# Kernel optimization log

Hardware: AMD Instinct MI355X
Metric: run time of the kernel (lower is better)

## Reference

```python
import jax, jax.numpy as jnp
import numpy as np

B, S, D, H, DK, F = 8, 1024, 1024, 16, 64, 4096
EPS = 1e-5


def _layer_norm(x, g, b):
    mu = jnp.mean(x, axis=-1, keepdims=True)
    var = jnp.var(x, axis=-1, keepdims=True)
    return (x - mu) * jax.lax.rsqrt(var + EPS) * g + b


def setup_inputs() -> dict:
    key = jax.random.key(0)
    ks = jax.random.split(key, 16)
    s = lambda fan: 1.0 / np.sqrt(fan)
    return {
        "src": jax.random.normal(ks[0], (B, S, D), dtype=jnp.float32),
        "Wq": jax.random.uniform(ks[1], (H, D, DK), jnp.float32, -s(D), s(D)),
        "bq": jnp.zeros((H, DK), jnp.float32),
        "Wk": jax.random.uniform(ks[2], (H, D, DK), jnp.float32, -s(D), s(D)),
        "bk": jnp.zeros((H, DK), jnp.float32),
        "Wv": jax.random.uniform(ks[3], (H, D, DK), jnp.float32, -s(D), s(D)),
        "bv": jnp.zeros((H, DK), jnp.float32),
        "Wo": jax.random.uniform(ks[4], (H * DK, D), jnp.float32, -s(H * DK), s(H * DK)),
        "bo": jnp.zeros((D,), jnp.float32),
        "g1": jnp.ones((D,), jnp.float32),
        "be1": jnp.zeros((D,), jnp.float32),
        "W1": jax.random.uniform(ks[5], (D, F), jnp.float32, -s(D), s(D)),
        "b1": jnp.zeros((F,), jnp.float32),
        "W2": jax.random.uniform(ks[6], (F, D), jnp.float32, -s(F), s(F)),
        "b2": jnp.zeros((D,), jnp.float32),
        "g2": jnp.ones((D,), jnp.float32),
        "be2": jnp.zeros((D,), jnp.float32),
    }


def reference(src, Wq, bq, Wk, bk, Wv, bv, Wo, bo, g1, be1, W1, b1, W2, b2, g2, be2):
    # Per-head projections (vectorized over the Python head loop of the original)
    q = jnp.einsum("bsd,hdk->bhsk", src, Wq) + bq[:, None, :]
    k = jnp.einsum("bsd,hdk->bhsk", src, Wk) + bk[:, None, :]
    v = jnp.einsum("bsd,hdk->bhsk", src, Wv) + bv[:, None, :]
    scale = 1.0 / jnp.sqrt(jnp.asarray(DK, src.dtype))
    scores = jnp.einsum("bhsk,bhtk->bhst", q, k) * scale  # [B,H,S,S]
    attn = jax.nn.softmax(scores, axis=-1)
    o = jnp.einsum("bhst,bhtk->bhsk", attn, v)
    # torch.cat over heads on last dim -> [B,S,H*DK] with head-major feature order
    o = o.transpose(0, 2, 1, 3).reshape(B, S, H * DK)
    attn_out = o @ Wo + bo
    x = _layer_norm(src + attn_out, g1, be1)  # dropout inactive at inference
    ff = jax.nn.relu(x @ W1 + b1) @ W2 + b2
    return _layer_norm(x + ff, g2, be2)
```

## Files before the change

kernel.cpp:

```cpp
#include <hip/hip_runtime.h>

#define Bq 8
#define Sq 1024
#define Dq 1024
#define Hq 16
#define DKq 64
#define Fq 4096
#define TOK (Bq*Sq)

typedef unsigned short u16;
typedef unsigned int u32;
typedef __bf16 bf16x8 __attribute__((ext_vector_type(8)));
typedef float  f32x4  __attribute__((ext_vector_type(4)));

__device__ __forceinline__ float bf2f(u16 u) {
  u32 x = ((u32)u) << 16;
  float f; __builtin_memcpy(&f, &x, 4); return f;
}
__device__ __forceinline__ u16 f2bf(float f) {
  u32 u; __builtin_memcpy(&u, &f, 4);
  u += 0x7fffu + ((u >> 16) & 1u);
  return (u16)(u >> 16);
}
__device__ __forceinline__ void async16(const u16* g, u16* l) {
  __builtin_amdgcn_global_load_lds(
      (__attribute__((address_space(1))) void*)(g),
      (__attribute__((address_space(3))) void*)(l), 16, 0, 0);
}
__device__ __forceinline__ u16 load_in(const void* p, long idx, u32 fp32) {
  return fp32 ? f2bf(((const float*)p)[idx]) : ((const u16*)p)[idx];
}
__device__ __forceinline__ int swzb(int row, int colb) {
  return row * 128 + (colb ^ ((row & 7) << 4));
}

struct InTab { const void* p[17]; int n[17]; };

__global__ void detect_all(InTab tab, u32* flags) {
  __shared__ int sh[3][256];
  int bi = blockIdx.x;
  const u16* buf = (const u16*)tab.p[bi];
  long n = tab.n[bi];
  long m = n < 65536 ? n : 65536;
  int t = threadIdx.x;
  int nanpat = 0, evz = 0, oddnz = 0;
  for (long i = t; i < m; i += 256) {
    u16 v = buf[i];
    if ((v & 0x7F80u) == 0x7F80u) nanpat++;
    if ((i & 1) == 0) { if (v == 0) evz++; }
    else { if (v != 0) oddnz++; }
  }
  sh[0][t] = nanpat; sh[1][t] = evz; sh[2][t] = oddnz;
  __syncthreads();
  for (int s = 128; s > 0; s >>= 1) {
    if (t < s) { sh[0][t] += sh[0][t+s]; sh[1][t] += sh[1][t+s]; sh[2][t] += sh[2][t+s]; }
    __syncthreads();
  }
  if (t == 0) {
    long half = m / 2;
    bool fp32 = (sh[0][0] > 8) ||
                (sh[1][0] > (half * 9) / 10 && sh[2][0] > (half * 9) / 10);
    flags[bi] = fp32 ? 1u : 0u;
  }
}

__global__ void diag_ws_too_small(u16* out, float code) { out[0] = f2bf(code); }

__global__ void diag_mixed(const u32* flags, void* out) {
  u32 a = flags[0];
  if (flags[1] != a || flags[7] != a || flags[11] != a || flags[13] != a) {
    if (a) ((float*)out)[0] = 3000.0f;
    else ((u16*)out)[0] = f2bf(3000.0f);
  }
}

__global__ __launch_bounds__(256) void pack_all(const void* __restrict__ Wq,
                                                const void* __restrict__ Wk,
                                                const void* __restrict__ Wv,
                                                const void* __restrict__ Wo,
                                                const void* __restrict__ W1,
                                                const void* __restrict__ W2,
                                                u16* __restrict__ Wqkv_t,
                                                u16* __restrict__ Wo_t,
                                                u16* __restrict__ W1_t,
                                                u16* __restrict__ W2_t,
                                                const u32* __restrict__ flags) {
  int id = blockIdx.x;
  const void* in; u16* out; u32 f; int R, C; long zin; int r0, c0;
  if (id < 768) {
    int w = id >> 8, t = id & 255;
    int z = t >> 4, xt = t & 15;
    in = (w == 0) ? Wq : ((w == 1) ? Wk : Wv);
    f = flags[(w == 0) ? 1 : ((w == 1) ? 3 : 5)];
    R = 1024; C = 64;
    zin = (long)z * 65536;
    out = Wqkv_t + (long)w * 1048576 + (long)z * 65536;
    r0 = xt * 64; c0 = 0;
  } else if (id < 1024) {
    int t = id - 768; int xt = t & 15, yt = t >> 4;
    in = Wo; f = flags[7]; R = 1024; C = 1024; zin = 0; out = Wo_t;
    r0 = xt * 64; c0 = yt * 64;
  } else if (id < 2048) {
    int t = id - 1024; int xt = t & 15, yt = t >> 4;
    in = W1; f = flags[11]; R = 1024; C = 4096; zin = 0; out = W1_t;
    r0 = xt * 64; c0 = yt * 64;
  } else {
    int t = id - 2048; int xt = t & 63, yt = t >> 6;
    in = W2; f = flags[13]; R = 4096; C = 1024; zin = 0; out = W2_t;
    r0 = xt * 64; c0 = yt * 64;
  }
  __shared__ u16 tile[64][65];
  int tx = threadIdx.x & 63, ty = threadIdx.x >> 6;
#pragma unroll
  for (int it = 0; it < 16; it++) {
    int row = it * 4 + ty;
    tile[row][tx] = load_in(in, zin + (long)(r0 + row) * C + (c0 + tx), f);
  }
  __syncthreads();
#pragma unroll
  for (int it = 0; it < 16; it++) {
    int cc = it * 4 + ty;
    out[(long)(c0 + cc) * R + r0 + tx] = tile[tx][cc];
  }
}

struct CvtTab { const void* p[10]; int flagidx[10]; int dstoff[10]; int n[10]; };
__global__ void cvt_small(CvtTab tab, u16* __restrict__ dst, const u32* __restrict__ flags) {
  int e = blockIdx.x;
  u32 f = flags[tab.flagidx[e]];
  const void* p = tab.p[e];
  int n = tab.n[e], o = tab.dstoff[e];
  for (int i = threadIdx.x; i < n; i += 256) dst[o + i] = load_in(p, i, f);
}

__global__ __launch_bounds__(256) void cvt_src(const void* __restrict__ in,
                                               u16* __restrict__ out,
                                               const u32* __restrict__ flag) {
  u32 f = *flag;
  long i8 = ((long)blockIdx.x * 256 + threadIdx.x) * 8;
  if (f) {
    const float4* f4 = (const float4*)((const float*)in + i8);
    float4 a = f4[0], b = f4[1];
    u16 v[8] = {f2bf(a.x), f2bf(a.y), f2bf(a.z), f2bf(a.w),
                f2bf(b.x), f2bf(b.y), f2bf(b.z), f2bf(b.w)};
    *(uint4*)(out + i8) = *(const uint4*)v;
  } else {
    *(uint4*)(out + i8) = *(const uint4*)((const u16*)in + i8);
  }
}

__global__ __launch_bounds__(256) void gemm_bt(const u16* __restrict__ A,
                                               const u16* __restrict__ Bt,
                                               const u16* __restrict__ bias,
                                               u16* __restrict__ C,
                                               int M, int N, int K, int act) {
  __shared__ alignas(16) u16 sA[2][128 * 32];
  __shared__ alignas(16) u16 sB[2][128 * 32];
  const int tid = threadIdx.x;
  const int wv = tid >> 6, lane = tid & 63;
  const int m16 = lane & 15, quad = lane >> 4;
  const long bm = (long)blockIdx.x * 128;
  const long bn = (long)blockIdx.y * 128;
  const int wm = (wv >> 1) * 64, wn = (wv & 1) * 64;

  f32x4 acc[4][4];
#pragma unroll
  for (int i = 0; i < 4; i++)
#pragma unroll
    for (int j = 0; j < 4; j++) acc[i][j] = (f32x4){0.f, 0.f, 0.f, 0.f};

  const int row_s = tid >> 2;
  const int col_s = (tid & 3) * 8;
  const u16* gA0 = A + (bm + row_s) * (long)K + col_s;
  const u16* gA1 = gA0 + 64 * (long)K;
  const u16* gB0 = Bt + (bn + row_s) * (long)K + col_s;
  const u16* gB1 = gB0 + 64 * (long)K;

  auto stage = [&](int p, int k) {
    async16(gA0 + k, &sA[p][wv * 512]);
    async16(gA1 + k, &sA[p][2048 + wv * 512]);
    async16(gB0 + k, &sB[p][wv * 512]);
    async16(gB1 + k, &sB[p][2048 + wv * 512]);
  };
  auto compute = [&](int p) {
    bf16x8 af[4], bf_[4];
#pragma unroll
    for (int mi = 0; mi < 4; mi++)
      af[mi] = *(const bf16x8*)&sA[p][(wm + mi * 16 + m16) * 32 + quad * 8];
#pragma unroll
    for (int ni = 0; ni < 4; ni++)
      bf_[ni] = *(const bf16x8*)&sB[p][(wn + ni * 16 + m16) * 32 + quad * 8];
#pragma unroll
    for (int mi = 0; mi < 4; mi++)
#pragma unroll
      for (int ni = 0; ni < 4; ni++)
        acc[mi][ni] = __builtin_amdgcn_mfma_f32_16x16x32_bf16(af[mi], bf_[ni], acc[mi][ni], 0, 0, 0);
  };

  stage(0, 0);
  for (int k0 = 0; k0 < K; k0 += 64) {
    __syncthreads();
    if (k0 + 32 < K) stage(1, k0 + 32);
    compute(0);
    __syncthreads();
    if (k0 + 64 < K) stage(0, k0 + 64);
    compute(1);
  }

  float bv4[4];
#pragma unroll
  for (int ni = 0; ni < 4; ni++) bv4[ni] = bf2f(bias[bn + wn + ni * 16 + m16]);

#pragma unroll
  for (int mi = 0; mi < 4; mi++) {
#pragma unroll
    for (int ni = 0; ni < 4; ni++) {
      long col = bn + wn + ni * 16 + m16;
#pragma unroll
      for (int r = 0; r < 4; r++) {
        long row = bm + wm + mi * 16 + quad * 4 + r;
        float v = acc[mi][ni][r] + bv4[ni];
        if (act) v = fmaxf(v, 0.f);
        C[row * N + col] = f2bf(v);
      }
    }
  }
}

#define MF16 __builtin_amdgcn_mfma_f32_16x16x32_bf16

#define TILE256(BUF, NBUF, DOA, DOB, KA, KB, VMS)                              \
  {                                                                            \
                   \
    _Pragma("unroll") for (int mi = 0; mi < 4; mi++)                           \
      _Pragma("unroll") for (int kk = 0; kk < 2; kk++)                         \
        afr[mi][kk] = *(const bf16x8*)&sA[BUF][offA + mi * 1024 + kof[kk]];    \
    _Pragma("unroll") for (int ni = 0; ni < 2; ni++)                           \
      _Pragma("unroll") for (int kk = 0; kk < 2; kk++)                         \
        bfr[ni][kk] = *(const bf16x8*)&sB[BUF][offB + ni * 1024 + kof[kk]];    \
    if (DOA) stA(NBUF, 0, KA);                                                 \
    __builtin_amdgcn_s_barrier();                                              \
    __builtin_amdgcn_s_setprio(1);                                             \
    _Pragma("unroll") for (int kk = 0; kk < 2; kk++)                           \
      _Pragma("unroll") for (int mi = 0; mi < 4; mi++)                         \
        _Pragma("unroll") for (int ni = 0; ni < 2; ni++)                       \
          acc[mi][ni] = MF16(afr[mi][kk], bfr[ni][kk], acc[mi][ni], 0, 0, 0);  \
    __builtin_amdgcn_s_setprio(0);                                             \
    __builtin_amdgcn_s_barrier();                                              \
                                 \
    _Pragma("unroll") for (int ni = 0; ni < 2; ni++)                           \
      _Pragma("unroll") for (int kk = 0; kk < 2; kk++)                         \
        bfr[2 + ni][kk] = *(const bf16x8*)&sB[BUF][offB + (2 + ni) * 1024 + kof[kk]]; \
    if (DOA) stA(NBUF, 1, KA);                                                 \
    __builtin_amdgcn_s_barrier();                                              \
    __builtin_amdgcn_s_setprio(1);                                             \
    _Pragma("unroll") for (int kk = 0; kk < 2; kk++)                           \
      _Pragma("unroll") for (int mi = 0; mi < 4; mi++)                         \
        _Pragma("unroll") for (int ni = 0; ni < 2; ni++)                       \
          acc[mi][2 + ni] = MF16(afr[mi][kk], bfr[2 + ni][kk], acc[mi][2 + ni], 0, 0, 0); \
    __builtin_amdgcn_s_setprio(0);                                             \
    __builtin_amdgcn_s_barrier();                                              \
     \
    _Pragma("unroll") for (int mi = 0; mi < 4; mi++)                           \
      _Pragma("unroll") for (int kk = 0; kk < 2; kk++)                         \
        afr[mi][kk] = *(const bf16x8*)&sA[BUF][offA + (4 + mi) * 1024 + kof[kk]]; \
    if (DOB) stB(BUF, 0, KB);                                                  \
    __builtin_amdgcn_s_barrier();                                              \
    __builtin_amdgcn_s_setprio(1);                                             \
    _Pragma("unroll") for (int kk = 0; kk < 2; kk++)                           \
      _Pragma("unroll") for (int mi = 0; mi < 4; mi++)                         \
        _Pragma("unroll") for (int ni = 0; ni < 2; ni++)                       \
          acc[4 + mi][2 + ni] = MF16(afr[mi][kk], bfr[2 + ni][kk], acc[4 + mi][2 + ni], 0, 0, 0); \
    __builtin_amdgcn_s_setprio(0);                                             \
    __builtin_amdgcn_s_barrier();                                              \
           \
    if (DOB) stB(BUF, 1, KB);                                                  \
    asm volatile("s_waitcnt vmcnt(" VMS ")" ::: "memory");                     \
    __builtin_amdgcn_s_barrier();                                              \
    __builtin_amdgcn_s_setprio(1);                                             \
    _Pragma("unroll") for (int kk = 0; kk < 2; kk++)                           \
      _Pragma("unroll") for (int mi = 0; mi < 4; mi++)                         \
        _Pragma("unroll") for (int ni = 0; ni < 2; ni++)                       \
          acc[4 + mi][ni] = MF16(afr[mi][kk], bfr[ni][kk], acc[4 + mi][ni], 0, 0, 0); \
    __builtin_amdgcn_s_setprio(0);                                             \
    __builtin_amdgcn_s_barrier();                                              \
  }

__global__ __launch_bounds__(512, 2) void gemm256(const u16* __restrict__ A,
                                                  const u16* __restrict__ Bt,
                                                  const u16* __restrict__ bias,
                                                  u16* __restrict__ C,
                                                  int M, int N, int K, int act,
                                                  int ldc, u16* __restrict__ Vt,
                                                  int mode) {
  __shared__ alignas(16) u16 sA[2][16384];
  __shared__ alignas(16) u16 sB[2][16384];
  const int tid = threadIdx.x;
  const int wv = tid >> 6, lane = tid & 63;
  const int m16 = lane & 15, quad = lane >> 4;
  const int wr = wv >> 2, wc = wv & 3;

  const int NT = N >> 8;
  int bid = blockIdx.x;
  {
    const int nwg = gridDim.x;
    const int q = nwg >> 3, r = nwg & 7;
    const int xcd = bid & 7, lp = bid >> 3;
    bid = (xcd < r ? xcd * (q + 1) : r * (q + 1) + (xcd - r) * q) + lp;
  }
  const long bm = (long)(bid / NT) * 256;
  const long bn = (long)(bid % NT) * 256;

  const int r0 = wv * 16 + (lane >> 3);
  const int cstg = ((lane & 7) ^ (lane >> 3)) * 8;
  const u16* gA0 = A  + (bm + r0) * (long)K + cstg;
  const u16* gA1 = A  + (bm + 128 + r0) * (long)K + cstg;
  const u16* gB0 = Bt + (bn + r0) * (long)K + cstg;
  const u16* gB1 = Bt + (bn + 128 + r0) * (long)K + cstg;
  const long k8 = 8 * (long)K;

  auto stA = [&](int nb, int h, int k0) {
    const u16* s = (h ? gA1 : gA0) + k0;
    u16* d = &sA[nb][h * 8192 + wv * 1024];
    async16(s, d);
    async16(s + k8, d + 512);
  };
  auto stB = [&](int nb, int h, int k0) {
    const u16* s = (h ? gB1 : gB0) + k0;
    u16* d = &sB[nb][h * 8192 + wv * 1024];
    async16(s, d);
    async16(s + k8, d + 512);
  };

  const int qs = quad ^ (m16 & 3);
  const int hb = (m16 >> 2) & 1;
  const int kof[2] = {hb * 32, 32 - hb * 32};
  const int offA = wr * 8192 + m16 * 64 + qs * 8;
  const int offB = (wc >> 1) * 8192 + (wc & 1) * 4096 + m16 * 64 + qs * 8;

  f32x4 acc[8][4];
#pragma unroll
  for (int i = 0; i < 8; i++)
#pragma unroll
    for (int j = 0; j < 4; j++) acc[i][j] = (f32x4){0.f, 0.f, 0.f, 0.f};
  bf16x8 afr[4][2], bfr[4][2];

  const int KT = K >> 6;

  stA(0, 0, 0); stA(0, 1, 0); stB(0, 0, 0); stB(0, 1, 0);
  stB(1, 0, 64); stB(1, 1, 64);
  asm volatile("s_waitcnt vmcnt(4)" ::: "memory");
  __builtin_amdgcn_s_barrier();

  int T = 0;
  for (; T + 2 < KT; T += 2) {
    const int kA1 = (T + 1) << 6, kB2 = (T + 2) << 6, kB3 = (T + 3) << 6;
    TILE256(0, 1, true, true, kA1, kB2, "4");
    TILE256(1, 0, true, true, kB2, kB3, "4");
  }
  {
    const int kA1 = (T + 1) << 6;
    TILE256(0, 1, true, false, kA1, 0, "0");
    TILE256(1, 0, false, false, 0, 0, "0");
  }

  float bv4[4];
#pragma unroll
  for (int ni = 0; ni < 4; ni++) bv4[ni] = bf2f(bias[bn + wc * 64 + ni * 16 + m16]);

#pragma unroll
  for (int mi = 0; mi < 8; mi++) {
#pragma unroll
    for (int ni = 0; ni < 4; ni++) {
      long col = bn + wc * 64 + ni * 16 + m16;
      long rowb = bm + wr * 128 + mi * 16 + quad * 4;
      if (mode == 1 && col >= 2048) {
        int hh = ((int)col >> 6) & 15, dk = (int)col & 63;
        int bb = (int)(rowb >> 10), ss = (int)(rowb & 1023);
        u16 t4[4];
#pragma unroll
        for (int r = 0; r < 4; r++) t4[r] = f2bf(acc[mi][ni][r] + bv4[ni]);
        *(uint2*)&Vt[(((long)bb * 16 + hh) * 64 + dk) * 1024 + ss] = *(const uint2*)t4;
      } else {
#pragma unroll
        for (int r = 0; r < 4; r++) {
          float v = acc[mi][ni][r] + bv4[ni];
          if (act) v = fmaxf(v, 0.f);
          C[(rowb + r) * (long)ldc + col] = f2bf(v);
        }
      }
    }
  }
}

__global__ __launch_bounds__(256, 4) void attn_fwd(const u16* __restrict__ qk,
                                                   const u16* __restrict__ Vt,
                                                   u16* __restrict__ attnO) {
  __shared__ alignas(16) u16 sQP[8192];
  __shared__ alignas(16) u16 sK[4096];
  __shared__ alignas(16) u16 sVt[4096];
  const int tid = threadIdx.x;
  const int bh = blockIdx.x;
  const int qt = blockIdx.y;
  const int b = bh >> 4, h = bh & 15;
  const int wv = tid >> 6, lane = tid & 63;
  const int m16 = lane & 15, quad = lane >> 4;
  const int kk = tid >> 3;
  const int t7 = tid & 7;

  char* cQP = (char*)sQP;
  char* cK = (char*)sK;
  char* cV = (char*)sVt;

  {
    int row = tid >> 1, half = tid & 1;
    const u16* g = qk + (long)(b * Sq + qt * 128 + row) * 2048 + h * 64 + half * 32;
#pragma unroll
    for (int j = 0; j < 4; j++) {
      uint4 raw = *(const uint4*)(g + j * 8);
      const u16* pv = (const u16*)&raw;
      u16 t[8];
#pragma unroll
      for (int e = 0; e < 8; e++) t[e] = f2bf(bf2f(pv[e]) * 0.125f);
      *(uint4*)(cQP + swzb(row, half * 64 + j * 16)) = *(const uint4*)t;
    }
  }
  __syncthreads();
  bf16x8 qf[2][2];
#pragma unroll
  for (int qt2 = 0; qt2 < 2; qt2++)
#pragma unroll
    for (int s = 0; s < 2; s++)
      qf[qt2][s] = *(const bf16x8*)(cQP + swzb(wv * 32 + qt2 * 16 + m16, s * 64 + quad * 16));

  f32x4 o[4][2];
#pragma unroll
  for (int dt = 0; dt < 4; dt++)
#pragma unroll
    for (int qt2 = 0; qt2 < 2; qt2++) o[dt][qt2] = (f32x4){0.f, 0.f, 0.f, 0.f};
  float mrun[2] = {-1e30f, -1e30f}, lrun[2] = {0.f, 0.f};

  const u16* gK = qk + (long)(b * Sq + kk) * 2048 + 1024 + h * 64 + t7 * 8;
  const u16* gV = Vt + ((long)bh * 64 + kk) * 1024 + t7 * 8;
  const long stepK = (long)64 * 2048;
  const int off0 = swzb(kk, t7 * 16);
  const int off1 = off0 + 4096;

  uint4 rk0 = *(const uint4*)gK;
  uint4 rk1 = *(const uint4*)(gK + 32 * 2048);
  uint4 rv0 = *(const uint4*)gV;
  uint4 rv1 = *(const uint4*)(gV + 32 * 1024);

  for (int kt = 0; kt < 16; kt++) {
    __syncthreads();
    *(uint4*)(cK + off0) = rk0;
    *(uint4*)(cK + off1) = rk1;
    *(uint4*)(cV + off0) = rv0;
    *(uint4*)(cV + off1) = rv1;
    __syncthreads();

    f32x4 st[4][2];
#pragma unroll
    for (int kt2 = 0; kt2 < 4; kt2++)
#pragma unroll
      for (int qt2 = 0; qt2 < 2; qt2++) st[kt2][qt2] = (f32x4){0.f, 0.f, 0.f, 0.f};
    __builtin_amdgcn_s_setprio(1);
#pragma unroll
    for (int s = 0; s < 2; s++) {
      bf16x8 kf[4];
#pragma unroll
      for (int kt2 = 0; kt2 < 4; kt2++)
        kf[kt2] = *(const bf16x8*)(cK + swzb(kt2 * 16 + m16, s * 64 + quad * 16));
#pragma unroll
      for (int kt2 = 0; kt2 < 4; kt2++)
#pragma unroll
        for (int qt2 = 0; qt2 < 2; qt2++)
          st[kt2][qt2] = MF16(kf[kt2], qf[qt2][s], st[kt2][qt2], 0, 0, 0);
    }
    __builtin_amdgcn_s_setprio(0);

    if (kt < 15) {
      rk0 = *(const uint4*)(gK + (long)(kt + 1) * stepK);
      rk1 = *(const uint4*)(gK + (long)(kt + 1) * stepK + 32 * 2048);
      rv0 = *(const uint4*)(gV + (kt + 1) * 64);
      rv1 = *(const uint4*)(gV + (kt + 1) * 64 + 32 * 1024);
    }

    char* cP = cQP + wv * 4096;
#pragma unroll
    for (int qt2 = 0; qt2 < 2; qt2++) {
      float pm = st[0][qt2][0];
#pragma unroll
      for (int kt2 = 0; kt2 < 4; kt2++)
#pragma unroll
        for (int r = 0; r < 4; r++) pm = fmaxf(pm, st[kt2][qt2][r]);
      pm = fmaxf(pm, __shfl_xor(pm, 16));
      pm = fmaxf(pm, __shfl_xor(pm, 32));
      float mnew = fmaxf(mrun[qt2], pm);
      float al = __expf(mrun[qt2] - mnew);
      mrun[qt2] = mnew;
      float rs = 0.f;
#pragma unroll
      for (int kt2 = 0; kt2 < 4; kt2++) {
        u16 t4[4];
#pragma unroll
        for (int r = 0; r < 4; r++) {
          float p = __expf(st[kt2][qt2][r] - mnew);
          rs += p;
          t4[r] = f2bf(p);
        }
        *(uint2*)(cP + swzb(qt2 * 16 + m16, kt2 * 32 + quad * 8)) = *(const uint2*)t4;
      }
      rs += __shfl_xor(rs, 16);
      rs += __shfl_xor(rs, 32);
      lrun[qt2] = lrun[qt2] * al + rs;
#pragma unroll
      for (int dt = 0; dt < 4; dt++)
#pragma unroll
        for (int r = 0; r < 4; r++) o[dt][qt2][r] *= al;
    }

    bf16x8 pb[2][2];
#pragma unroll
    for (int qt2 = 0; qt2 < 2; qt2++)
#pragma unroll
      for (int ks = 0; ks < 2; ks++)
        pb[qt2][ks] = *(const bf16x8*)(cP + swzb(qt2 * 16 + m16, ks * 64 + quad * 16));
    __builtin_amdgcn_s_setprio(1);
#pragma unroll
    for (int dt = 0; dt < 4; dt++) {
      bf16x8 v0 = *(const bf16x8*)(cV + swzb(dt * 16 + m16, quad * 16));
      bf16x8 v1 = *(const bf16x8*)(cV + swzb(dt * 16 + m16, 64 + quad * 16));
#pragma unroll
      for (int qt2 = 0; qt2 < 2; qt2++) {
        o[dt][qt2] = MF16(v0, pb[qt2][0], o[dt][qt2], 0, 0, 0);
        o[dt][qt2] = MF16(v1, pb[qt2][1], o[dt][qt2], 0, 0, 0);
      }
    }
    __builtin_amdgcn_s_setprio(0);
  }

#pragma unroll
  for (int qt2 = 0; qt2 < 2; qt2++) {
    float rl = 1.f / lrun[qt2];
    long tok = (long)(b * Sq + qt * 128 + wv * 32 + qt2 * 16 + m16);
#pragma unroll
    for (int dt = 0; dt < 4; dt++) {
      u16 t4[4];
#pragma unroll
      for (int r = 0; r < 4; r++) t4[r] = f2bf(o[dt][qt2][r] * rl);
      *(uint2*)&attnO[tok * 1024 + h * 64 + dt * 16 + quad * 4] = *(const uint2*)t4;
    }
  }
}

__global__ __launch_bounds__(256) void add_ln(const u16* __restrict__ X,
                                              const u16* __restrict__ Y,
                                              const u16* __restrict__ g,
                                              const u16* __restrict__ be,
                                              u16* __restrict__ out) {
  const int row = blockIdx.x;
  const int t = threadIdx.x;
  const long base = (long)row * Dq;
  float v[4]; float s = 0.f, ss = 0.f;
#pragma unroll
  for (int i = 0; i < 4; i++) {
    int idx = i * 256 + t;
    float x = bf2f(X[base + idx]) + bf2f(Y[base + idx]);
    v[i] = x; s += x; ss += x * x;
  }
#pragma unroll
  for (int off = 32; off > 0; off >>= 1) { s += __shfl_down(s, off); ss += __shfl_down(ss, off); }
  __shared__ float red[8];
  int wv = t >> 6, ln = t & 63;
  if (ln == 0) { red[wv] = s; red[4 + wv] = ss; }
  __syncthreads();
  s = red[0] + red[1] + red[2] + red[3];
  ss = red[4] + red[5] + red[6] + red[7];
  float mean = s * (1.f / Dq);
  float var = ss * (1.f / Dq) - mean * mean;
  float rstd = rsqrtf(var + 1e-5f);
#pragma unroll
  for (int i = 0; i < 4; i++) {
    int idx = i * 256 + t;
    float o = (v[i] - mean) * rstd * bf2f(g[idx]) + bf2f(be[idx]);
    out[base + idx] = f2bf(o);
  }
}

__global__ __launch_bounds__(256) void add_ln_out(const u16* __restrict__ X,
                                                  const u16* __restrict__ Y,
                                                  const u16* __restrict__ g,
                                                  const u16* __restrict__ be,
                                                  void* __restrict__ out,
                                                  const u32* __restrict__ outflag) {
  const u32 fp32 = *outflag;
  const int row = blockIdx.x;
  const int t = threadIdx.x;
  const long base = (long)row * Dq;
  float v[4]; float s = 0.f, ss = 0.f;
#pragma unroll
  for (int i = 0; i < 4; i++) {
    int idx = i * 256 + t;
    float x = bf2f(X[base + idx]) + bf2f(Y[base + idx]);
    v[i] = x; s += x; ss += x * x;
  }
#pragma unroll
  for (int off = 32; off > 0; off >>= 1) { s += __shfl_down(s, off); ss += __shfl_down(ss, off); }
  __shared__ float red[8];
  int wv = t >> 6, ln = t & 63;
  if (ln == 0) { red[wv] = s; red[4 + wv] = ss; }
  __syncthreads();
  s = red[0] + red[1] + red[2] + red[3];
  ss = red[4] + red[5] + red[6] + red[7];
  float mean = s * (1.f / Dq);
  float var = ss * (1.f / Dq) - mean * mean;
  float rstd = rsqrtf(var + 1e-5f);
#pragma unroll
  for (int i = 0; i < 4; i++) {
    int idx = i * 256 + t;
    float o = (v[i] - mean) * rstd * bf2f(g[idx]) + bf2f(be[idx]);
    if (fp32) ((float*)out)[base + idx] = o;
    else ((u16*)out)[base + idx] = f2bf(o);
  }
}

extern "C" void kernel_launch(void* const* d_in, const int* in_sizes, int n_in,
                              void* d_out, int out_size, void* d_ws, size_t ws_size,
                              hipStream_t stream) {
  char* ws = (char*)d_ws;
  size_t off = 0;
  auto alloc = [&](size_t bytes) {
    void* p = ws + off;
    off += (bytes + 255) & ~(size_t)255;
    return p;
  };
  u32* flags  = (u32*)alloc(32 * 4);
  u16* Wqkv_t = (u16*)alloc((size_t)3072 * 1024 * 2);
  u16* Wo_t   = (u16*)alloc((size_t)1024 * 1024 * 2);
  u16* W1_t   = (u16*)alloc((size_t)4096 * 1024 * 2);
  u16* W2_t   = (u16*)alloc((size_t)1024 * 4096 * 2);
  u16* svec   = (u16*)alloc((size_t)13312 * 2);
  u16* src_bf = (u16*)alloc((size_t)TOK * 1024 * 2);
  u16* regA   = (u16*)alloc((size_t)TOK * 4096 * 2);
  size_t need_chunk2 = off;
  size_t need_full   = off + (size_t)TOK * 4096 * 2 / 2;

  u16* outw = (u16*)d_out;
  int CH;
  if (ws_size >= need_full) { CH = 8192; (void)alloc((size_t)32 << 20); }
  else if (ws_size >= need_chunk2) CH = 4096;
  else if (ws_size >= need_chunk2 - ((size_t)16 << 20)) CH = 2048;
  else {
    diag_ws_too_small<<<1, 1, 0, stream>>>(outw, 8000.0f + (float)(ws_size >> 20));
    return;
  }

  u16* qk    = regA;
  u16* Vt    = regA + (size_t)TOK * 2048;
  u16* attnb = regA + (size_t)TOK * 3072;
  u16* proj  = regA;
  u16* x     = regA + (size_t)TOK * 1024;
  u16* h1    = regA + (size_t)TOK * 2048;
  u16* f2    = src_bf;

  u16* bqkv = svec + 0;
  u16* bo_c = svec + 3072;
  u16* g1_c = svec + 4096;
  u16* be1_c = svec + 5120;
  u16* b1_c = svec + 6144;
  u16* b2_c = svec + 10240;
  u16* g2_c = svec + 11264;
  u16* be2_c = svec + 12288;

  InTab itab;
  for (int i = 0; i < 17; i++) { itab.p[i] = d_in[i]; itab.n[i] = in_sizes[i]; }
  detect_all<<<dim3(17), 256, 0, stream>>>(itab, flags);

  pack_all<<<dim3(3072), 256, 0, stream>>>(d_in[1], d_in[3], d_in[5], d_in[7], d_in[11], d_in[13],
                                           Wqkv_t, Wo_t, W1_t, W2_t, flags);

  CvtTab ct;
  const int srcs[10] = {2, 4, 6, 8, 9, 10, 12, 14, 15, 16};
  const int offs[10] = {0, 1024, 2048, 3072, 4096, 5120, 6144, 10240, 11264, 12288};
  const int lens[10] = {1024, 1024, 1024, 1024, 1024, 1024, 4096, 1024, 1024, 1024};
  for (int e = 0; e < 10; e++) { ct.p[e] = d_in[srcs[e]]; ct.flagidx[e] = srcs[e]; ct.dstoff[e] = offs[e]; ct.n[e] = lens[e]; }
  cvt_small<<<dim3(10), 256, 0, stream>>>(ct, svec, flags);

  cvt_src<<<dim3(TOK * 1024 / (256 * 8)), 256, 0, stream>>>(d_in[0], src_bf, &flags[0]);

  gemm256<<<dim3(32 * 12), 512, 0, stream>>>(src_bf, Wqkv_t, bqkv, qk, TOK, 3072, 1024, 0,
                                             2048, Vt, 1);
  attn_fwd<<<dim3(128, 8), 256, 0, stream>>>(qk, Vt, attnb);
  gemm_bt<<<dim3(64, 8), 256, 0, stream>>>(attnb, Wo_t, bo_c, proj, TOK, 1024, 1024, 0);
  add_ln<<<dim3(TOK), 256, 0, stream>>>(src_bf, proj, g1_c, be1_c, x);
  for (int c = 0; c < TOK / CH; c++) {
    const u16* xc = x + (size_t)c * CH * 1024;
    u16* f2c = f2 + (size_t)c * CH * 1024;
    if (CH >= 4096) {
      gemm256<<<dim3((CH / 256) * 16), 512, 0, stream>>>(xc, W1_t, b1_c, h1, CH, 4096, 1024, 1,
                                                         4096, nullptr, 0);
    } else {
      gemm_bt<<<dim3(CH / 128, 32), 256, 0, stream>>>(xc, W1_t, b1_c, h1, CH, 4096, 1024, 1);
    }
    gemm_bt<<<dim3(CH / 128, 8), 256, 0, stream>>>(h1, W2_t, b2_c, f2c, CH, 1024, 4096, 0);
  }
  add_ln_out<<<dim3(TOK), 256, 0, stream>>>(x, f2, g2_c, be2_c, d_out, &flags[0]);
  diag_mixed<<<1, 1, 0, stream>>>(flags, d_out);
}
```

Before: 585.1 us.

## Add 256x128-tile double-buffered GEMM for output and FFN2 projections

Adds a 512-thread GEMM kernel with 256x128 output tiles, double-buffered LDS with async global-to-LDS loads, XCD-aware block remapping and setprio around the MFMA bursts. It replaces the 128-tile gemm_bt for the attention output projection and, when the chunk size is 8192, for the FFN second GEMM. The larger tiles raise data reuse and cut grid size for N=1024 GEMMs. The cost is fewer blocks (256), which may underfill the CUs, and the FFN2 path only runs if CH equals 8192.

```diff
diff --git a/kernel.cpp b/kernel.cpp
--- a/kernel.cpp
+++ b/kernel.cpp
@@ -393,6 +393,134 @@
   }
 }
 
+#define TILE128(BUF, NBUF, DOA, DOB, KA, KB, VMS)                              \
+  {                                                                            \
+                           \
+    _Pragma("unroll") for (int mi = 0; mi < 4; mi++)                           \
+      _Pragma("unroll") for (int kk = 0; kk < 2; kk++)                         \
+        afr[mi][kk] = *(const bf16x8*)&sA[BUF][offA + mi * 1024 + kof[kk]];    \
+    _Pragma("unroll") for (int ni = 0; ni < 2; ni++)                           \
+      _Pragma("unroll") for (int kk = 0; kk < 2; kk++)                         \
+        bfr[ni][kk] = *(const bf16x8*)&sB[BUF][offB + ni * 1024 + kof[kk]];    \
+    if (DOA) stA(NBUF, 0, KA);                                                 \
+    __builtin_amdgcn_s_barrier();                                              \
+    __builtin_amdgcn_s_setprio(1);                                             \
+    _Pragma("unroll") for (int kk = 0; kk < 2; kk++)                           \
+      _Pragma("unroll") for (int mi = 0; mi < 4; mi++)                         \
+        _Pragma("unroll") for (int ni = 0; ni < 2; ni++)                       \
+          acc[mi][ni] = MF16(afr[mi][kk], bfr[ni][kk], acc[mi][ni], 0, 0, 0);  \
+    __builtin_amdgcn_s_setprio(0);                                             \
+    __builtin_amdgcn_s_barrier();                                              \
+                            \
+    _Pragma("unroll") for (int ni = 0; ni < 2; ni++)                           \
+      _Pragma("unroll") for (int kk = 0; kk < 2; kk++)                         \
+        bfr[2 + ni][kk] = *(const bf16x8*)&sB[BUF][offB + (2 + ni) * 1024 + kof[kk]]; \
+    if (DOA) stA(NBUF, 1, KA);                                                 \
+    __builtin_amdgcn_s_barrier();                                              \
+    __builtin_amdgcn_s_setprio(1);                                             \
+    _Pragma("unroll") for (int kk = 0; kk < 2; kk++)                           \
+      _Pragma("unroll") for (int mi = 0; mi < 4; mi++)                         \
+        _Pragma("unroll") for (int ni = 0; ni < 2; ni++)                       \
+          acc[mi][2 + ni] = MF16(afr[mi][kk], bfr[2 + ni][kk], acc[mi][2 + ni], 0, 0, 0); \
+    __builtin_amdgcn_s_setprio(0);                                             \
+    __builtin_amdgcn_s_barrier();                                              \
+                   \
+    if (DOB) stB(BUF, KB);                                                     \
+    asm volatile("s_waitcnt vmcnt(" VMS ")" ::: "memory");                     \
+    __builtin_amdgcn_s_barrier();                                              \
+  }
+
+__global__ __launch_bounds__(512, 2) void gemm256x128(const u16* __restrict__ A,
+                                                      const u16* __restrict__ Bt,
+                                                      const u16* __restrict__ bias,
+                                                      u16* __restrict__ C,
+                                                      int M, int N, int K, int act) {
+  __shared__ alignas(16) u16 sA[2][16384];
+  __shared__ alignas(16) u16 sB[2][8192];
+  const int tid = threadIdx.x;
+  const int wv = tid >> 6, lane = tid & 63;
+  const int m16 = lane & 15, quad = lane >> 4;
+  const int wr = wv >> 1, wc = wv & 1;
+
+  const int NT = N >> 7;
+  int bid = blockIdx.x;
+  {
+    const int nwg = gridDim.x;
+    const int q = nwg >> 3, r = nwg & 7;
+    const int xcd = bid & 7, lp = bid >> 3;
+    bid = (xcd < r ? xcd * (q + 1) : r * (q + 1) + (xcd - r) * q) + lp;
+  }
+  const long bm = (long)(bid / NT) * 256;
+  const long bn = (long)(bid % NT) * 128;
+
+  const int r0 = wv * 16 + (lane >> 3);
+  const int cstg = ((lane & 7) ^ (lane >> 3)) * 8;
+  const u16* gA0 = A + (bm + r0) * (long)K + cstg;
+  const u16* gA1 = A + (bm + 128 + r0) * (long)K + cstg;
+  const u16* gB0 = Bt + (bn + r0) * (long)K + cstg;
+  const long k8 = 8 * (long)K;
+
+  auto stA = [&](int nb, int h, int k0) {
+    const u16* s = (h ? gA1 : gA0) + k0;
+    u16* d = &sA[nb][h * 8192 + wv * 1024];
+    async16(s, d);
+    async16(s + k8, d + 512);
+  };
+  auto stB = [&](int nb, int k0) {
+    const u16* s = gB0 + k0;
+    u16* d = &sB[nb][wv * 1024];
+    async16(s, d);
+    async16(s + k8, d + 512);
+  };
+
+  const int qs = quad ^ (m16 & 3);
+  const int hb = (m16 >> 2) & 1;
+  const int kof[2] = {hb * 32, 32 - hb * 32};
+  const int offA = (wr >> 1) * 8192 + (wr & 1) * 4096 + m16 * 64 + qs * 8;
+  const int offB = wc * 4096 + m16 * 64 + qs * 8;
+
+  f32x4 acc[4][4];
+#pragma unroll
+  for (int i = 0; i < 4; i++)
+#pragma unroll
+    for (int j = 0; j < 4; j++) acc[i][j] = (f32x4){0.f, 0.f, 0.f, 0.f};
+  bf16x8 afr[4][2], bfr[4][2];
+
+  const int KT = K >> 6;
+
+  stA(0, 0, 0); stA(0, 1, 0); stB(0, 0);
+  stB(1, 64);
+  asm volatile("s_waitcnt vmcnt(2)" ::: "memory");
+  __builtin_amdgcn_s_barrier();
+
+  int T = 0;
+  for (; T + 2 < KT; T += 2) {
+    TILE128(0, 1, true, true, (T + 1) << 6, (T + 2) << 6, "2");
+    TILE128(1, 0, true, true, (T + 2) << 6, (T + 3) << 6, "2");
+  }
+  TILE128(0, 1, true, false, (T + 1) << 6, 0, "0");
+  TILE128(1, 0, false, false, 0, 0, "0");
+
+  float bv4[4];
+#pragma unroll
+  for (int ni = 0; ni < 4; ni++) bv4[ni] = bf2f(bias[bn + wc * 64 + ni * 16 + m16]);
+
+#pragma unroll
+  for (int mi = 0; mi < 4; mi++) {
+#pragma unroll
+    for (int ni = 0; ni < 4; ni++) {
+      long col = bn + wc * 64 + ni * 16 + m16;
+      long rowb = bm + wr * 64 + mi * 16 + quad * 4;
+#pragma unroll
+      for (int r = 0; r < 4; r++) {
+        float v = acc[mi][ni][r] + bv4[ni];
+        if (act) v = fmaxf(v, 0.f);
+        C[(rowb + r) * (long)N + col] = f2bf(v);
+      }
+    }
+  }
+}
+
 __global__ __launch_bounds__(256, 4) void attn_fwd(const u16* __restrict__ qk,
                                                    const u16* __restrict__ Vt,
                                                    u16* __restrict__ attnO) {
@@ -692,7 +820,7 @@
   gemm256<<<dim3(32 * 12), 512, 0, stream>>>(src_bf, Wqkv_t, bqkv, qk, TOK, 3072, 1024, 0,
                                              2048, Vt, 1);
   attn_fwd<<<dim3(128, 8), 256, 0, stream>>>(qk, Vt, attnb);
-  gemm_bt<<<dim3(64, 8), 256, 0, stream>>>(attnb, Wo_t, bo_c, proj, TOK, 1024, 1024, 0);
+  gemm256x128<<<dim3(256), 512, 0, stream>>>(attnb, Wo_t, bo_c, proj, TOK, 1024, 1024, 0);
   add_ln<<<dim3(TOK), 256, 0, stream>>>(src_bf, proj, g1_c, be1_c, x);
   for (int c = 0; c < TOK / CH; c++) {
     const u16* xc = x + (size_t)c * CH * 1024;
@@ -703,7 +831,11 @@
     } else {
       gemm_bt<<<dim3(CH / 128, 32), 256, 0, stream>>>(xc, W1_t, b1_c, h1, CH, 4096, 1024, 1);
     }
-    gemm_bt<<<dim3(CH / 128, 8), 256, 0, stream>>>(h1, W2_t, b2_c, f2c, CH, 1024, 4096, 0);
+    if (CH == 8192) {
+      gemm256x128<<<dim3((CH / 256) * 8), 512, 0, stream>>>(h1, W2_t, b2_c, f2c, CH, 1024, 4096, 0);
+    } else {
+      gemm_bt<<<dim3(CH / 128, 8), 256, 0, stream>>>(h1, W2_t, b2_c, f2c, CH, 1024, 4096, 0);
+    }
   }
   add_ln_out<<<dim3(TOK), 256, 0, stream>>>(x, f2, g2_c, be2_c, d_out, &flags[0]);
   diag_mixed<<<1, 1, 0, stream>>>(flags, d_out);
```

New measurement: 573.0 us. -2.1%, faster.
